# Kernel optimization log

Measured on AMD Instinct MI355X. Metric: run time of the kernel, lower is better.

Reference implementation:

```python
import jax, jax.numpy as jnp
import numpy as np

N_NODES = 50000
N_EDGES = 800000
N_GRAPHS = 64
IN_DIM = 128
HID = 128
S, C = 4, 16
DIM1 = 3 * S * S  # 48
OUT_DIM = DIM1 * C  # 768


def gcn_conv(x, W, b, src, dst, w):
    """PyG GCNConv: linear transform, then sym-normalized aggregation with self-loops (weight 1)."""
    n = x.shape[0]
    h = x @ W  # [N, out]
    deg = jnp.zeros((n,), x.dtype).at[dst].add(w) + 1.0  # self-loop weight 1
    dinv = jax.lax.rsqrt(deg)
    norm = dinv[src] * w * dinv[dst]  # [E]
    agg = jnp.zeros_like(h).at[dst].add(h[src] * norm[:, None])
    agg = agg + h * (1.0 / deg)[:, None]  # self-loop messages
    return agg + b


def setup_inputs() -> dict:
    key = jax.random.key(0)
    ks = jax.random.split(key, 16)
    x = jax.random.normal(ks[0], (N_NODES, IN_DIM), jnp.float32)
    edge_index = jax.random.randint(ks[1], (2, N_EDGES), 0, N_NODES, jnp.int64)
    edge_attr = jax.random.uniform(ks[2], (N_EDGES,), jnp.float32)
    batch = jnp.sort(jax.random.randint(ks[3], (N_NODES,), 0, N_GRAPHS, jnp.int64))

    def glorot(k, fan_in, fan_out):
        s = np.sqrt(6.0 / (fan_in + fan_out)).astype(np.float32)
        return jax.random.uniform(k, (fan_in, fan_out), jnp.float32, -s, s)

    return {
        "x": x, "edge_index": edge_index, "edge_attr": edge_attr, "batch": batch,
        "W1": glorot(ks[4], IN_DIM, HID), "b1": jnp.zeros((HID,), jnp.float32),
        "W2": glorot(ks[5], HID, HID // 2), "b2": jnp.zeros((HID // 2,), jnp.float32),
        "W3": glorot(ks[6], HID // 2, HID // 4), "b3": jnp.zeros((HID // 4,), jnp.float32),
        "Wl": glorot(ks[7], HID // 4, OUT_DIM), "bl": jnp.zeros((OUT_DIM,), jnp.float32),
    }


def reference(x, edge_index, edge_attr, batch, W1, b1, W2, b2, W3, b3, Wl, bl):
    src, dst = edge_index[0], edge_index[1]
    w = edge_attr / edge_attr.max()
    h = jax.nn.relu(gcn_conv(x, W1, b1, src, dst, w))
    h = jax.nn.relu(gcn_conv(h, W2, b2, src, dst, w))
    h = jax.nn.relu(gcn_conv(h, W3, b3, src, dst, w))
    # global mean pool over graphs
    sums = jax.ops.segment_sum(h, batch, num_segments=N_GRAPHS)
    cnt = jax.ops.segment_sum(jnp.ones((h.shape[0],), h.dtype), batch, num_segments=N_GRAPHS)
    pooled = sums / jnp.maximum(cnt, 1.0)[:, None]
    out = pooled @ Wl + bl  # [G, OUT_DIM]
    return out.reshape(N_GRAPHS, DIM1, C)
```

## Files before the change

### kernel.cpp

```cpp
#include <hip/hip_runtime.h>
#include <hip/hip_bf16.h>

#define NN 50000
#define NE 800000
#define NG 64
#define OUTD 768

#define G1B ((NN + 63) / 64)
#define MAXB 128
#define SSEG 64
#define TTL 8
#define ESEG (NE / SSEG)
#define NTL (NN / TTL)
#define HRB (SSEG * TTL)

__device__ __forceinline__ float bflo(unsigned int u) { return __uint_as_float(u << 16); }
__device__ __forceinline__ float bfhi(unsigned int u) { return __uint_as_float(u & 0xffff0000u); }
__device__ __forceinline__ unsigned short f2bf(float f) {
    unsigned int u = __float_as_uint(f);
    return (unsigned short)((u + 0x7fffu + ((u >> 16) & 1u)) >> 16);
}
__device__ __forceinline__ unsigned int pack2bf(float lo, float hi) {
    return (unsigned int)f2bf(lo) | ((unsigned int)f2bf(hi) << 16);
}

typedef __attribute__((ext_vector_type(8))) short bf16x8;
typedef __attribute__((ext_vector_type(4))) float f32x4;
union FragU { uint4 u4; bf16x8 v; };

template <int K, int N>
constexpr int mfma_lds_bytes() { return (K / 32) * (N / 16) * 1024; }

template <int K, int N, typename TX>
__device__ __forceinline__ void mfma_gemm_body(char* smem,
                                               const TX* __restrict__ X,
                                               const float* __restrict__ W,
                                               unsigned short* __restrict__ Y,
                                               int nRows, int bx) {
    constexpr int NCT = N / 16;
    constexpr int KS = K / 32;
    const int tid = threadIdx.x;

    for (int q = tid; q < KS * NCT * 64; q += 256) {
        int lane = q & 63;
        int fi = q >> 6;
        int ct = fi % NCT, kc = fi / NCT;
        int col = ct * 16 + (lane & 15);
        int kb = kc * 32 + ((lane >> 4) << 3);
        uint4 w;
        w.x = pack2bf(W[(size_t)(kb + 0) * N + col], W[(size_t)(kb + 1) * N + col]);
        w.y = pack2bf(W[(size_t)(kb + 2) * N + col], W[(size_t)(kb + 3) * N + col]);
        w.z = pack2bf(W[(size_t)(kb + 4) * N + col], W[(size_t)(kb + 5) * N + col]);
        w.w = pack2bf(W[(size_t)(kb + 6) * N + col], W[(size_t)(kb + 7) * N + col]);
        *(uint4*)(smem + (size_t)q * 16) = w;
    }
    __syncthreads();

    const int lane = tid & 63;
    const int wv = tid >> 6;
    const int m = lane & 15;
    const int quad = lane >> 4;
    const int row = bx * 64 + wv * 16 + m;
    const bool rowok = row < nRows;
    const TX* xr = X + (size_t)(rowok ? row : 0) * K;

    f32x4 acc[NCT];
#pragma unroll
    for (int ct = 0; ct < NCT; ++ct) acc[ct] = (f32x4){0.f, 0.f, 0.f, 0.f};

#pragma unroll
    for (int kc = 0; kc < KS; ++kc) {
        const int k0 = kc * 32 + quad * 8;
        FragU a;
        if constexpr (sizeof(TX) == 4) {
            float4 a0 = make_float4(0.f, 0.f, 0.f, 0.f), a1 = a0;
            if (rowok) {
                a0 = *(const float4*)(xr + k0);
                a1 = *(const float4*)(xr + k0 + 4);
            }
            a.u4 = make_uint4(pack2bf(a0.x, a0.y), pack2bf(a0.z, a0.w),
                              pack2bf(a1.x, a1.y), pack2bf(a1.z, a1.w));
        } else {
            a.u4 = rowok ? *(const uint4*)(xr + k0) : make_uint4(0, 0, 0, 0);
        }
#pragma unroll
        for (int ct = 0; ct < NCT; ++ct) {
            FragU b;
            b.u4 = *(const uint4*)(smem + ((size_t)(kc * NCT + ct) * 64 + lane) * 16);
            acc[ct] = __builtin_amdgcn_mfma_f32_16x16x32_bf16(a.v, b.v, acc[ct], 0, 0, 0);
        }
    }

    const int orowb = bx * 64 + wv * 16 + quad * 4;
#pragma unroll
    for (int ct = 0; ct < NCT; ++ct) {
        int col = ct * 16 + m;
#pragma unroll
        for (int r = 0; r < 4; ++r) {
            int orow = orowb + r;
            if (orow < nRows) Y[(size_t)orow * N + col] = f2bf(acc[ct][r]);
        }
    }
}

template <int K, int N, typename TX>
__global__ __launch_bounds__(256) void mfma_gemm_kernel(const TX* __restrict__ X,
                                                        const float* __restrict__ W,
                                                        unsigned short* __restrict__ Y,
                                                        int nRows) {
    extern __shared__ char smem[];
    mfma_gemm_body<K, N>(smem, X, W, Y, nRows, blockIdx.x);
}

__global__ __launch_bounds__(256) void fused1_kernel(const float* __restrict__ x,
                                                     const float* __restrict__ W1,
                                                     unsigned short* __restrict__ bufA,
                                                     const float* __restrict__ ea,
                                                     unsigned int* wmax,
                                                     const int* __restrict__ dst,
                                                     int* __restrict__ rank,
                                                     unsigned short* __restrict__ pcnt) {
    extern __shared__ char smem[];
    const int b = blockIdx.x;
    if (b < G1B) {
        mfma_gemm_body<128, 128>(smem, x, W1, bufA, NN, b);
    } else if (b < G1B + MAXB) {
        float* red = (float*)smem;
        const int bb = b - G1B;
        float m = 0.0f;
        for (int i = bb * 256 + threadIdx.x; i < NE; i += MAXB * 256)
            m = fmaxf(m, ea[i]);
        red[threadIdx.x] = m;
        __syncthreads();
        for (int off = 128; off > 0; off >>= 1) {
            if (threadIdx.x < off)
                red[threadIdx.x] = fmaxf(red[threadIdx.x], red[threadIdx.x + off]);
            __syncthreads();
        }
        if (threadIdx.x == 0) atomicMax(wmax, __float_as_uint(red[0]));
    } else {
        const int b2 = b - G1B - MAXB;
        const int seg = b2 >> 3;
        const int tile = b2 & 7;
        int* lcnt = (int*)smem;
        for (int i = threadIdx.x; i < NTL; i += 256) lcnt[i] = 0;
        __syncthreads();
        const int base = seg * ESEG;
        const int nlo = tile * NTL;
        for (int e = base + threadIdx.x; e < base + ESEG; e += 256) {
            int d = dst[e] - nlo;
            if ((unsigned)d < (unsigned)NTL)
                rank[e] = atomicAdd(&lcnt[d], 1);
        }
        __syncthreads();
        unsigned short* prow = pcnt + (size_t)seg * NN + nlo;
        for (int i = threadIdx.x; i < NTL; i += 256)
            prow[i] = (unsigned short)lcnt[i];
    }
}

__global__ __launch_bounds__(256) void comb_kernel(unsigned short* __restrict__ pcnt,
                                                   int* __restrict__ hist,
                                                   int* __restrict__ blocksum) {
    __shared__ int red[256];
    int n = blockIdx.x * 256 + threadIdx.x;
    int run = 0;
    if (n < NN) {
#pragma unroll
        for (int s = 0; s < SSEG; ++s) {
            size_t idx = (size_t)s * NN + n;
            int v = pcnt[idx];
            pcnt[idx] = (unsigned short)run;
            run += v;
        }
        hist[n] = run;
    }
    red[threadIdx.x] = (n < NN) ? run : 0;
    __syncthreads();
    for (int off = 128; off > 0; off >>= 1) {
        if (threadIdx.x < off) red[threadIdx.x] += red[threadIdx.x + off];
        __syncthreads();
    }
    if (threadIdx.x == 0) blocksum[blockIdx.x] = red[0];
}

__global__ __launch_bounds__(256) void scan2_kernel(const int* __restrict__ blocksum,
                                                    int* __restrict__ blockoff,
                                                    int* __restrict__ total_out, int nb) {
    __shared__ int s[256];
    const int tid = threadIdx.x;
    int v = (tid < nb) ? blocksum[tid] : 0;
    s[tid] = v;
    __syncthreads();
    for (int off = 1; off < 256; off <<= 1) {
        int t = (tid >= off) ? s[tid - off] : 0;
        __syncthreads();
        s[tid] += t;
        __syncthreads();
    }
    if (tid < nb) blockoff[tid] = s[tid] - v;
    if (tid == nb - 1) *total_out = s[tid];
}

__global__ __launch_bounds__(256) void scan3_kernel(const int* __restrict__ hist,
                                                    const int* __restrict__ blockoff,
                                                    int* __restrict__ rowptr, int n) {
    __shared__ int s[256];
    const int tid = threadIdx.x;
    int i = blockIdx.x * 256 + tid;
    int v = (i < n) ? hist[i] : 0;
    s[tid] = v;
    __syncthreads();
    for (int off = 1; off < 256; off <<= 1) {
        int t = (tid >= off) ? s[tid - off] : 0;
        __syncthreads();
        s[tid] += t;
        __syncthreads();
    }
    if (i < n) rowptr[i] = blockoff[blockIdx.x] + s[tid] - v;
}

__global__ void scat_kernel(const int* __restrict__ src, const int* __restrict__ dst,
                            const float* __restrict__ ea,
                            const int* __restrict__ rowptr,
                            const unsigned short* __restrict__ pcnt,
                            const int* __restrict__ rank,
                            int2* __restrict__ epack, int nE) {
    int e = blockIdx.x * blockDim.x + threadIdx.x;
    if (e >= nE) return;
    int s = e / ESEG;
    int d = dst[e];
    int pos = rowptr[d] + (int)pcnt[(size_t)s * NN + d] + rank[e];
    epack[pos] = make_int2(src[e], __float_as_int(ea[e]));
}

__global__ void deg_kernel(const int2* __restrict__ epack, const int* __restrict__ rowptr,
                           const unsigned int* __restrict__ wmax,
                           float* __restrict__ dinv, float* __restrict__ invdeg, int n) {
    int i = blockIdx.x * blockDim.x + threadIdx.x;
    if (i >= n) return;
    float rw = 1.0f / __uint_as_float(*wmax);
    int s0 = rowptr[i], s1 = rowptr[i + 1];
    float s = 0.f;
    for (int e = s0; e < s1; ++e) s += __int_as_float(epack[e].y);
    float d = fmaf(s, rw, 1.0f);
    dinv[i] = rsqrtf(d);
    invdeg[i] = 1.0f / d;
}

__global__ void coef_kernel(int2* __restrict__ epack, const int* __restrict__ rowptr,
                            const float* __restrict__ dinv,
                            const unsigned int* __restrict__ wmax, int n) {
    int i = blockIdx.x * blockDim.x + threadIdx.x;
    if (i >= n) return;
    float rw = 1.0f / __uint_as_float(*wmax);
    float di = dinv[i];
    int s0 = rowptr[i], s1 = rowptr[i + 1];
    for (int e = s0; e < s1; ++e) {
        int2 p = epack[e];
        p.y = __float_as_int(dinv[p.x] * (__int_as_float(p.y) * rw) * di);
        epack[e] = p;
    }
}

template <int D>
__global__ __launch_bounds__(256) void agg_kernel(const unsigned short* __restrict__ H,
                                                  const int* __restrict__ rowptr,
                                                  const int2* __restrict__ epack,
                                                  const float* __restrict__ invdeg,
                                                  const float* __restrict__ bias,
                                                  unsigned short* __restrict__ out,
                                                  int nNodes) {
    constexpr int LPE = D / 8;
    constexpr int EPW = 64 / LPE;
    const int lane = threadIdx.x & 63;
    const int n = (blockIdx.x << 2) | (threadIdx.x >> 6);
    if (n >= nNodes) return;
    const int esub = lane / LPE;
    const int f8 = (lane % LPE) * 8;
    const int s0 = rowptr[n];
    const int cnt = rowptr[n + 1] - s0;

    float a[8] = {};
    int kb = 0;
    for (; kb + 2 * EPW <= cnt; kb += 2 * EPW) {
        const int2 pa = epack[s0 + kb + esub];
        const int2 pb = epack[s0 + kb + EPW + esub];
        const uint4 ua = *(const uint4*)(H + (size_t)pa.x * D + f8);
        const uint4 ub = *(const uint4*)(H + (size_t)pb.x * D + f8);
        const float ca = __int_as_float(pa.y);
        const float cb = __int_as_float(pb.y);
        a[0] = fmaf(ca, bflo(ua.x), a[0]); a[1] = fmaf(ca, bfhi(ua.x), a[1]);
        a[2] = fmaf(ca, bflo(ua.y), a[2]); a[3] = fmaf(ca, bfhi(ua.y), a[3]);
        a[4] = fmaf(ca, bflo(ua.z), a[4]); a[5] = fmaf(ca, bfhi(ua.z), a[5]);
        a[6] = fmaf(ca, bflo(ua.w), a[6]); a[7] = fmaf(ca, bfhi(ua.w), a[7]);
        a[0] = fmaf(cb, bflo(ub.x), a[0]); a[1] = fmaf(cb, bfhi(ub.x), a[1]);
        a[2] = fmaf(cb, bflo(ub.y), a[2]); a[3] = fmaf(cb, bfhi(ub.y), a[3]);
        a[4] = fmaf(cb, bflo(ub.z), a[4]); a[5] = fmaf(cb, bfhi(ub.z), a[5]);
        a[6] = fmaf(cb, bflo(ub.w), a[6]); a[7] = fmaf(cb, bfhi(ub.w), a[7]);
    }
    for (; kb < cnt; kb += EPW) {
        const int idx = kb + esub;
        const bool ok = idx < cnt;
        const int2 p = ok ? epack[s0 + idx] : make_int2(n, 0);
        const uint4 u = *(const uint4*)(H + (size_t)p.x * D + f8);
        const float c = ok ? __int_as_float(p.y) : 0.f;
        a[0] = fmaf(c, bflo(u.x), a[0]); a[1] = fmaf(c, bfhi(u.x), a[1]);
        a[2] = fmaf(c, bflo(u.y), a[2]); a[3] = fmaf(c, bfhi(u.y), a[3]);
        a[4] = fmaf(c, bflo(u.z), a[4]); a[5] = fmaf(c, bfhi(u.z), a[5]);
        a[6] = fmaf(c, bflo(u.w), a[6]); a[7] = fmaf(c, bfhi(u.w), a[7]);
    }
#pragma unroll
    for (int off = LPE; off < 64; off <<= 1) {
#pragma unroll
        for (int j = 0; j < 8; ++j) a[j] += __shfl_xor(a[j], off);
    }
    if (esub == 0) {
        const float id = invdeg[n];
        const uint4 un = *(const uint4*)(H + (size_t)n * D + f8);
        const float4 b0 = *(const float4*)(bias + f8);
        const float4 b1 = *(const float4*)(bias + f8 + 4);
        float o[8];
        o[0] = fmaxf(fmaf(id, bflo(un.x), a[0]) + b0.x, 0.f);
        o[1] = fmaxf(fmaf(id, bfhi(un.x), a[1]) + b0.y, 0.f);
        o[2] = fmaxf(fmaf(id, bflo(un.y), a[2]) + b0.z, 0.f);
        o[3] = fmaxf(fmaf(id, bfhi(un.y), a[3]) + b0.w, 0.f);
        o[4] = fmaxf(fmaf(id, bflo(un.z), a[4]) + b1.x, 0.f);
        o[5] = fmaxf(fmaf(id, bfhi(un.z), a[5]) + b1.y, 0.f);
        o[6] = fmaxf(fmaf(id, bflo(un.w), a[6]) + b1.z, 0.f);
        o[7] = fmaxf(fmaf(id, bfhi(un.w), a[7]) + b1.w, 0.f);
        uint4 w;
        w.x = pack2bf(o[0], o[1]);
        w.y = pack2bf(o[2], o[3]);
        w.z = pack2bf(o[4], o[5]);
        w.w = pack2bf(o[6], o[7]);
        *(uint4*)(out + (size_t)n * D + f8) = w;
    }
}

__global__ __launch_bounds__(256) void pool2_kernel(const unsigned short* __restrict__ h,
                                                    const int* __restrict__ batch,
                                                    float* __restrict__ pooled, int n) {
    const int g = blockIdx.x;
    int lo = 0, hi = n;
    while (lo < hi) { int m = (lo + hi) >> 1; if (batch[m] < g) lo = m + 1; else hi = m; }
    const int start = lo;
    lo = start; hi = n;
    while (lo < hi) { int m = (lo + hi) >> 1; if (batch[m] < g + 1) lo = m + 1; else hi = m; }
    const int end = lo;

    __shared__ float part[256];
    const int f = threadIdx.x & 31;
    const int r = threadIdx.x >> 5;
    float acc = 0.f;
    for (int i = start + r; i < end; i += 8)
        acc += __uint_as_float((unsigned int)h[(size_t)i * 32 + f] << 16);
    part[threadIdx.x] = acc;
    __syncthreads();
    if (threadIdx.x < 32) {
        float s = 0.f;
#pragma unroll
        for (int q = 0; q < 8; ++q) s += part[q * 32 + f];
        float inv = 1.0f / fmaxf((float)(end - start), 1.0f);
        pooled[g * 32 + f] = s * inv;
    }
}

__global__ void final_kernel(const float* __restrict__ pooled,
                             const float* __restrict__ Wl, const float* __restrict__ bl,
                             float* __restrict__ out) {
    int idx = blockIdx.x * blockDim.x + threadIdx.x;
    int g = idx / OUTD, o = idx - g * OUTD;
    float acc = bl[o];
#pragma unroll
    for (int k = 0; k < 32; ++k)
        acc = fmaf(pooled[g * 32 + k], Wl[k * OUTD + o], acc);
    out[idx] = acc;
}

extern "C" void kernel_launch(void* const* d_in, const int* in_sizes, int n_in,
                              void* d_out, int out_size, void* d_ws, size_t ws_size,
                              hipStream_t stream) {
    const float* x = (const float*)d_in[0];
    const int* eidx = (const int*)d_in[1];
    const float* ea = (const float*)d_in[2];
    const int* batch = (const int*)d_in[3];
    const float* W1 = (const float*)d_in[4];
    const float* b1 = (const float*)d_in[5];
    const float* W2 = (const float*)d_in[6];
    const float* b2 = (const float*)d_in[7];
    const float* W3 = (const float*)d_in[8];
    const float* b3 = (const float*)d_in[9];
    const float* Wl = (const float*)d_in[10];
    const float* bl = (const float*)d_in[11];
    const int* src = eidx;
    const int* dst = eidx + NE;

    char* p = (char*)d_ws;
    auto take = [&](size_t bytes) {
        char* r = p;
        p += (bytes + 255) & ~(size_t)255;
        return r;
    };
    float* dinv = (float*)take(NN * 4);
    float* invdeg = (float*)take(NN * 4);
    int* hist = (int*)take(NN * 4);
    int* rowptr = (int*)take((NN + 1) * 4);
    int* blocksum = (int*)take(256 * 4);
    int* blockoff = (int*)take(256 * 4);
    int2* epack = (int2*)take((size_t)NE * 8);
    float* pooled = (float*)take(NG * 32 * 4);
    unsigned int* wmax = (unsigned int*)take(4);
    unsigned short* bufA = (unsigned short*)take((size_t)NN * 128 * 2);
    unsigned short* bufB = (unsigned short*)take((size_t)NN * 128 * 2);
    int* rank = (int*)bufB;
    unsigned short* pcnt = (unsigned short*)((char*)bufB + (size_t)NE * 4 + 256);

    const int nblk = (NN + 255) / 256;
    const int eblk = (NE + 255) / 256;

    hipMemsetAsync(wmax, 0, 4, stream);

    constexpr int LDS1 = mfma_lds_bytes<128, 128>();
    static_assert(LDS1 >= NTL * 4, "HR branch LDS must fit");
    fused1_kernel<<<G1B + MAXB + HRB, 256, LDS1, stream>>>(x, W1, bufA, ea, wmax,
                                                           dst, rank, pcnt);
    comb_kernel<<<nblk, 256, 0, stream>>>(pcnt, hist, blocksum);
    scan2_kernel<<<1, 256, 0, stream>>>(blocksum, blockoff, &rowptr[NN], nblk);
    scan3_kernel<<<nblk, 256, 0, stream>>>(hist, blockoff, rowptr, NN);
    scat_kernel<<<eblk, 256, 0, stream>>>(src, dst, ea, rowptr, pcnt, rank, epack, NE);
    deg_kernel<<<nblk, 256, 0, stream>>>(epack, rowptr, wmax, dinv, invdeg, NN);
    coef_kernel<<<nblk, 256, 0, stream>>>(epack, rowptr, dinv, wmax, NN);

    agg_kernel<128><<<(NN + 3) / 4, 256, 0, stream>>>(bufA, rowptr, epack, invdeg, b1, bufB, NN);
    mfma_gemm_kernel<128, 64, unsigned short>
        <<<G1B, 256, mfma_lds_bytes<128, 64>(), stream>>>(bufB, W2, bufA, NN);
    agg_kernel<64><<<(NN + 3) / 4, 256, 0, stream>>>(bufA, rowptr, epack, invdeg, b2, bufB, NN);
    mfma_gemm_kernel<64, 32, unsigned short>
        <<<G1B, 256, mfma_lds_bytes<64, 32>(), stream>>>(bufB, W3, bufA, NN);
    agg_kernel<32><<<(NN + 7) / 8 * 2, 256, 0, stream>>>(bufA, rowptr, epack, invdeg, b3, bufB, NN);

    pool2_kernel<<<NG, 256, 0, stream>>>(bufB, batch, pooled, NN);
    final_kernel<<<(NG * OUTD) / 256, 256, 0, stream>>>(pooled, Wl, bl, (float*)d_out);
}
```

Measured before the change: 294.4 us.

## Pack histogram counters, fuse scans, drop coef pass, fuse pool with final linear

The histogram stage now uses 16-bit packed LDS counters with fewer segments and tiles, and reads dst and edge weights as vectors. The two scan kernels merge into one that redundantly scans the block sums in every block. The per-edge coefficient rewrite pass is removed: each aggregation recomputes the normalization from a per-node factor, at the cost of an extra gather per edge in all three layers. Pooling and the final linear layer become one kernel, which cuts launches but runs the output GEMV on only 64 blocks.

```diff
diff --git a/kernel.cpp b/kernel.cpp
--- a/kernel.cpp
+++ b/kernel.cpp
@@ -8,8 +8,8 @@
 
 #define G1B ((NN + 63) / 64)
 #define MAXB 128
-#define SSEG 64
-#define TTL 8
+#define SSEG 32
+#define TTL 4
 #define ESEG (NE / SSEG)
 #define NTL (NN / TTL)
 #define HRB (SSEG * TTL)
@@ -127,9 +127,12 @@
     } else if (b < G1B + MAXB) {
         float* red = (float*)smem;
         const int bb = b - G1B;
+        const float4* ea4 = (const float4*)ea;
         float m = 0.0f;
-        for (int i = bb * 256 + threadIdx.x; i < NE; i += MAXB * 256)
-            m = fmaxf(m, ea[i]);
+        for (int i = bb * 256 + threadIdx.x; i < NE / 4; i += MAXB * 256) {
+            float4 v = ea4[i];
+            m = fmaxf(fmaxf(m, fmaxf(v.x, v.y)), fmaxf(v.z, v.w));
+        }
         red[threadIdx.x] = m;
         __syncthreads();
         for (int off = 128; off > 0; off >>= 1) {
@@ -140,22 +143,31 @@
         if (threadIdx.x == 0) atomicMax(wmax, __float_as_uint(red[0]));
     } else {
         const int b2 = b - G1B - MAXB;
-        const int seg = b2 >> 3;
-        const int tile = b2 & 7;
-        int* lcnt = (int*)smem;
-        for (int i = threadIdx.x; i < NTL; i += 256) lcnt[i] = 0;
+        const int seg = b2 >> 2;
+        const int tile = b2 & 3;
+        unsigned int* lcnt = (unsigned int*)smem;
+        for (int i = threadIdx.x; i < NTL / 2; i += 256) lcnt[i] = 0;
         __syncthreads();
         const int base = seg * ESEG;
         const int nlo = tile * NTL;
-        for (int e = base + threadIdx.x; e < base + ESEG; e += 256) {
-            int d = dst[e] - nlo;
-            if ((unsigned)d < (unsigned)NTL)
-                rank[e] = atomicAdd(&lcnt[d], 1);
-        }
-        __syncthreads();
-        unsigned short* prow = pcnt + (size_t)seg * NN + nlo;
-        for (int i = threadIdx.x; i < NTL; i += 256)
-            prow[i] = (unsigned short)lcnt[i];
+        const int4* dst4 = (const int4*)(dst + base);
+        for (int g = threadIdx.x; g < ESEG / 4; g += 256) {
+            const int4 v = dst4[g];
+            const int e0 = base + g * 4;
+            const int dd[4] = {v.x, v.y, v.z, v.w};
+#pragma unroll
+            for (int j = 0; j < 4; ++j) {
+                int d = dd[j] - nlo;
+                if ((unsigned)d < (unsigned)NTL) {
+                    unsigned sh = (unsigned)(d & 1) << 4;
+                    unsigned old = atomicAdd(&lcnt[d >> 1], 1u << sh);
+                    rank[e0 + j] = (int)((old >> sh) & 0xffffu);
+                }
+            }
+        }
+        __syncthreads();
+        unsigned int* prow32 = (unsigned int*)(pcnt + (size_t)seg * NN + nlo);
+        for (int i = threadIdx.x; i < NTL / 2; i += 256) prow32[i] = lcnt[i];
     }
 }
 
@@ -184,29 +196,24 @@
     if (threadIdx.x == 0) blocksum[blockIdx.x] = red[0];
 }
 
-__global__ __launch_bounds__(256) void scan2_kernel(const int* __restrict__ blocksum,
-                                                    int* __restrict__ blockoff,
-                                                    int* __restrict__ total_out, int nb) {
+__global__ __launch_bounds__(256) void scan3_kernel(const int* __restrict__ hist,
+                                                    const int* __restrict__ blocksum,
+                                                    int* __restrict__ rowptr, int n, int nb) {
+    __shared__ int sb[256];
     __shared__ int s[256];
     const int tid = threadIdx.x;
-    int v = (tid < nb) ? blocksum[tid] : 0;
-    s[tid] = v;
+    int bv = (tid < nb) ? blocksum[tid] : 0;
+    sb[tid] = bv;
     __syncthreads();
     for (int off = 1; off < 256; off <<= 1) {
-        int t = (tid >= off) ? s[tid - off] : 0;
-        __syncthreads();
-        s[tid] += t;
-        __syncthreads();
-    }
-    if (tid < nb) blockoff[tid] = s[tid] - v;
-    if (tid == nb - 1) *total_out = s[tid];
-}
-
-__global__ __launch_bounds__(256) void scan3_kernel(const int* __restrict__ hist,
-                                                    const int* __restrict__ blockoff,
-                                                    int* __restrict__ rowptr, int n) {
-    __shared__ int s[256];
-    const int tid = threadIdx.x;
+        int t = (tid >= off) ? sb[tid - off] : 0;
+        __syncthreads();
+        sb[tid] += t;
+        __syncthreads();
+    }
+    const int boff = (blockIdx.x > 0) ? sb[blockIdx.x - 1] : 0;
+    const int total = sb[nb - 1];
+
     int i = blockIdx.x * 256 + tid;
     int v = (i < n) ? hist[i] : 0;
     s[tid] = v;
@@ -217,7 +224,8 @@
         s[tid] += t;
         __syncthreads();
     }
-    if (i < n) rowptr[i] = blockoff[blockIdx.x] + s[tid] - v;
+    if (i < n) rowptr[i] = boff + s[tid] - v;
+    if (blockIdx.x == 0 && tid == 0) rowptr[n] = total;
 }
 
 __global__ void scat_kernel(const int* __restrict__ src, const int* __restrict__ dst,
@@ -236,31 +244,17 @@
 
 __global__ void deg_kernel(const int2* __restrict__ epack, const int* __restrict__ rowptr,
                            const unsigned int* __restrict__ wmax,
-                           float* __restrict__ dinv, float* __restrict__ invdeg, int n) {
+                           float* __restrict__ nrm, float* __restrict__ invdeg, int n) {
     int i = blockIdx.x * blockDim.x + threadIdx.x;
     if (i >= n) return;
     float rw = 1.0f / __uint_as_float(*wmax);
+    float srw = sqrtf(rw);
     int s0 = rowptr[i], s1 = rowptr[i + 1];
     float s = 0.f;
     for (int e = s0; e < s1; ++e) s += __int_as_float(epack[e].y);
     float d = fmaf(s, rw, 1.0f);
-    dinv[i] = rsqrtf(d);
+    nrm[i] = rsqrtf(d) * srw;
     invdeg[i] = 1.0f / d;
-}
-
-__global__ void coef_kernel(int2* __restrict__ epack, const int* __restrict__ rowptr,
-                            const float* __restrict__ dinv,
-                            const unsigned int* __restrict__ wmax, int n) {
-    int i = blockIdx.x * blockDim.x + threadIdx.x;
-    if (i >= n) return;
-    float rw = 1.0f / __uint_as_float(*wmax);
-    float di = dinv[i];
-    int s0 = rowptr[i], s1 = rowptr[i + 1];
-    for (int e = s0; e < s1; ++e) {
-        int2 p = epack[e];
-        p.y = __float_as_int(dinv[p.x] * (__int_as_float(p.y) * rw) * di);
-        epack[e] = p;
-    }
 }
 
 template <int D>
@@ -268,6 +262,7 @@
                                                   const int* __restrict__ rowptr,
                                                   const int2* __restrict__ epack,
                                                   const float* __restrict__ invdeg,
+                                                  const float* __restrict__ nrm,
                                                   const float* __restrict__ bias,
                                                   unsigned short* __restrict__ out,
                                                   int nNodes) {
@@ -280,6 +275,7 @@
     const int f8 = (lane % LPE) * 8;
     const int s0 = rowptr[n];
     const int cnt = rowptr[n + 1] - s0;
+    const float dn = nrm[n];
 
     float a[8] = {};
     int kb = 0;
@@ -288,8 +284,8 @@
         const int2 pb = epack[s0 + kb + EPW + esub];
         const uint4 ua = *(const uint4*)(H + (size_t)pa.x * D + f8);
         const uint4 ub = *(const uint4*)(H + (size_t)pb.x * D + f8);
-        const float ca = __int_as_float(pa.y);
-        const float cb = __int_as_float(pb.y);
+        const float ca = nrm[pa.x] * __int_as_float(pa.y) * dn;
+        const float cb = nrm[pb.x] * __int_as_float(pb.y) * dn;
         a[0] = fmaf(ca, bflo(ua.x), a[0]); a[1] = fmaf(ca, bfhi(ua.x), a[1]);
         a[2] = fmaf(ca, bflo(ua.y), a[2]); a[3] = fmaf(ca, bfhi(ua.y), a[3]);
         a[4] = fmaf(ca, bflo(ua.z), a[4]); a[5] = fmaf(ca, bfhi(ua.z), a[5]);
@@ -304,7 +300,7 @@
         const bool ok = idx < cnt;
         const int2 p = ok ? epack[s0 + idx] : make_int2(n, 0);
         const uint4 u = *(const uint4*)(H + (size_t)p.x * D + f8);
-        const float c = ok ? __int_as_float(p.y) : 0.f;
+        const float c = ok ? nrm[p.x] * __int_as_float(p.y) * dn : 0.f;
         a[0] = fmaf(c, bflo(u.x), a[0]); a[1] = fmaf(c, bfhi(u.x), a[1]);
         a[2] = fmaf(c, bflo(u.y), a[2]); a[3] = fmaf(c, bfhi(u.y), a[3]);
         a[4] = fmaf(c, bflo(u.z), a[4]); a[5] = fmaf(c, bfhi(u.z), a[5]);
@@ -338,9 +334,11 @@
     }
 }
 
-__global__ __launch_bounds__(256) void pool2_kernel(const unsigned short* __restrict__ h,
-                                                    const int* __restrict__ batch,
-                                                    float* __restrict__ pooled, int n) {
+__global__ __launch_bounds__(256) void poolfin_kernel(const unsigned short* __restrict__ h,
+                                                      const int* __restrict__ batch,
+                                                      const float* __restrict__ Wl,
+                                                      const float* __restrict__ bl,
+                                                      float* __restrict__ out, int n) {
     const int g = blockIdx.x;
     int lo = 0, hi = n;
     while (lo < hi) { int m = (lo + hi) >> 1; if (batch[m] < g) lo = m + 1; else hi = m; }
@@ -350,6 +348,7 @@
     const int end = lo;
 
     __shared__ float part[256];
+    __shared__ float spool[32];
     const int f = threadIdx.x & 31;
     const int r = threadIdx.x >> 5;
     float acc = 0.f;
@@ -362,20 +361,18 @@
 #pragma unroll
         for (int q = 0; q < 8; ++q) s += part[q * 32 + f];
         float inv = 1.0f / fmaxf((float)(end - start), 1.0f);
-        pooled[g * 32 + f] = s * inv;
-    }
-}
-
-__global__ void final_kernel(const float* __restrict__ pooled,
-                             const float* __restrict__ Wl, const float* __restrict__ bl,
-                             float* __restrict__ out) {
-    int idx = blockIdx.x * blockDim.x + threadIdx.x;
-    int g = idx / OUTD, o = idx - g * OUTD;
-    float acc = bl[o];
-#pragma unroll
-    for (int k = 0; k < 32; ++k)
-        acc = fmaf(pooled[g * 32 + k], Wl[k * OUTD + o], acc);
-    out[idx] = acc;
+        spool[f] = s * inv;
+    }
+    __syncthreads();
+#pragma unroll
+    for (int t = 0; t < 3; ++t) {
+        const int o = t * 256 + threadIdx.x;
+        float a2 = bl[o];
+#pragma unroll
+        for (int k = 0; k < 32; ++k)
+            a2 = fmaf(spool[k], Wl[k * OUTD + o], a2);
+        out[(size_t)g * OUTD + o] = a2;
+    }
 }
 
 extern "C" void kernel_launch(void* const* d_in, const int* in_sizes, int n_in,
@@ -402,14 +399,12 @@
         p += (bytes + 255) & ~(size_t)255;
         return r;
     };
-    float* dinv = (float*)take(NN * 4);
+    float* nrm = (float*)take(NN * 4);
     float* invdeg = (float*)take(NN * 4);
     int* hist = (int*)take(NN * 4);
     int* rowptr = (int*)take((NN + 1) * 4);
     int* blocksum = (int*)take(256 * 4);
-    int* blockoff = (int*)take(256 * 4);
     int2* epack = (int2*)take((size_t)NE * 8);
-    float* pooled = (float*)take(NG * 32 * 4);
     unsigned int* wmax = (unsigned int*)take(4);
     unsigned short* bufA = (unsigned short*)take((size_t)NN * 128 * 2);
     unsigned short* bufB = (unsigned short*)take((size_t)NN * 128 * 2);
@@ -422,24 +417,21 @@
     hipMemsetAsync(wmax, 0, 4, stream);
 
     constexpr int LDS1 = mfma_lds_bytes<128, 128>();
-    static_assert(LDS1 >= NTL * 4, "HR branch LDS must fit");
+    static_assert(LDS1 >= NTL * 2, "HR branch LDS (packed u16 counters) must fit");
     fused1_kernel<<<G1B + MAXB + HRB, 256, LDS1, stream>>>(x, W1, bufA, ea, wmax,
                                                            dst, rank, pcnt);
     comb_kernel<<<nblk, 256, 0, stream>>>(pcnt, hist, blocksum);
-    scan2_kernel<<<1, 256, 0, stream>>>(blocksum, blockoff, &rowptr[NN], nblk);
-    scan3_kernel<<<nblk, 256, 0, stream>>>(hist, blockoff, rowptr, NN);
+    scan3_kernel<<<nblk, 256, 0, stream>>>(hist, blocksum, rowptr, NN, nblk);
     scat_kernel<<<eblk, 256, 0, stream>>>(src, dst, ea, rowptr, pcnt, rank, epack, NE);
-    deg_kernel<<<nblk, 256, 0, stream>>>(epack, rowptr, wmax, dinv, invdeg, NN);
-    coef_kernel<<<nblk, 256, 0, stream>>>(epack, rowptr, dinv, wmax, NN);
-
-    agg_kernel<128><<<(NN + 3) / 4, 256, 0, stream>>>(bufA, rowptr, epack, invdeg, b1, bufB, NN);
+    deg_kernel<<<nblk, 256, 0, stream>>>(epack, rowptr, wmax, nrm, invdeg, NN);
+
+    agg_kernel<128><<<(NN + 3) / 4, 256, 0, stream>>>(bufA, rowptr, epack, invdeg, nrm, b1, bufB, NN);
     mfma_gemm_kernel<128, 64, unsigned short>
         <<<G1B, 256, mfma_lds_bytes<128, 64>(), stream>>>(bufB, W2, bufA, NN);
-    agg_kernel<64><<<(NN + 3) / 4, 256, 0, stream>>>(bufA, rowptr, epack, invdeg, b2, bufB, NN);
+    agg_kernel<64><<<(NN + 3) / 4, 256, 0, stream>>>(bufA, rowptr, epack, invdeg, nrm, b2, bufB, NN);
     mfma_gemm_kernel<64, 32, unsigned short>
         <<<G1B, 256, mfma_lds_bytes<64, 32>(), stream>>>(bufB, W3, bufA, NN);
-    agg_kernel<32><<<(NN + 7) / 8 * 2, 256, 0, stream>>>(bufA, rowptr, epack, invdeg, b3, bufB, NN);
-
-    pool2_kernel<<<NG, 256, 0, stream>>>(bufB, batch, pooled, NN);
-    final_kernel<<<(NG * OUTD) / 256, 256, 0, stream>>>(pooled, Wl, bl, (float*)d_out);
-}
+    agg_kernel<32><<<(NN + 7) / 8 * 2, 256, 0, stream>>>(bufA, rowptr, epack, invdeg, nrm, b3, bufB, NN);
+
+    poolfin_kernel<<<NG, 256, 0, stream>>>(bufB, batch, Wl, bl, (float*)d_out, NN);
+}
```

Result: faster. 271.3 us (-7.9%).
